# Kernel optimization log

Measured on AMD Instinct MI355X. Metric: run time of the kernel, lower is better.

## Reference

```python
import jax, jax.numpy as jnp
import numpy as np

N_NODES = 50000
N_EDGES = 800000
IN_DIM = 256
OUT_DIM = 64


def setup_inputs() -> dict:
    key = jax.random.key(0)
    k1, k2, k3, k4, k5 = jax.random.split(key, 5)
    h = jax.random.normal(k1, (N_NODES, IN_DIM), dtype=jnp.float32)
    # fc: Linear(in_dim, out_dim, bias=False) -> weight shape [out_dim, in_dim]
    W_fc = jax.random.normal(k2, (OUT_DIM, IN_DIM), dtype=jnp.float32) / np.sqrt(IN_DIM)
    # attn_fc: Linear(2*out_dim, 1, bias=False) -> weight shape [1, 2*out_dim]
    W_attn = jax.random.normal(k3, (1, 2 * OUT_DIM), dtype=jnp.float32) / np.sqrt(2 * OUT_DIM)
    src = jax.random.randint(k4, (N_EDGES,), 0, N_NODES, dtype=jnp.int64 if jax.config.read('jax_enable_x64') else jnp.int32).astype(jnp.int32)
    dst = jax.random.randint(k5, (N_EDGES,), 0, N_NODES, dtype=jnp.int32)
    return {"h": h, "W_fc": W_fc, "W_attn": W_attn, "src": src, "dst": dst}


def reference(h, W_fc, W_attn, src, dst):
    # z = self.fc(h)
    z = h @ W_fc.T                              # [N, D]
    # edge_attention: e = leaky_relu(attn_fc(cat(z_src, z_dst)))
    z_src = z[src]                              # [E, D] gather
    z_dst = z[dst]                              # [E, D] gather
    z2 = jnp.concatenate([z_src, z_dst], axis=1)  # [E, 2D]
    e = jax.nn.leaky_relu(z2 @ W_attn.T)[:, 0]  # [E], torch default slope 0.01
    # reduce_func: segment softmax over incoming edges per dst node
    n = h.shape[0]
    m = jax.ops.segment_max(e, dst, num_segments=n)        # [N] per-node max
    e_exp = jnp.exp(e - m[dst])                             # [E] stable exp
    denom = jax.ops.segment_sum(e_exp, dst, num_segments=n)  # [N]
    alpha = e_exp / jnp.maximum(denom, 1e-16)[dst]          # [E]
    # h' = sum_j alpha_ij * z_j
    out = jax.ops.segment_sum(alpha[:, None] * z_src, dst, num_segments=n)  # [N, D]
    return out
```

## Files before the change

### kernel.cpp

```cpp
#include <hip/hip_runtime.h>

#define N_NODES 50000
#define N_EDGES 800000
#define IN_DIM  256
#define OUT_DIM 64
#define BINW    128
#define NBINS   512
#define NBINS_USED ((N_NODES + BINW - 1) / BINW)
#define PB      112
#define CH4     ((N_EDGES / 4 + PB - 1) / PB)
#define NB_GEMM ((N_NODES + 63) / 64)
#define GRID_FUSED 896

typedef _Float16 f16;
typedef __attribute__((ext_vector_type(4))) _Float16 f16x4;
typedef __attribute__((ext_vector_type(8))) _Float16 f16x8;
typedef __attribute__((ext_vector_type(4))) float f32x4;


__global__ __launch_bounds__(256) void k_prep(const float* __restrict__ W,
                                              f16* __restrict__ Wh,
                                              int* __restrict__ binCount) {
    int idx = blockIdx.x * 256 + threadIdx.x;
    if (idx < (OUT_DIM * IN_DIM) / 4) {
        float4 v = ((const float4*)W)[idx];
        f16x4 p = { (f16)v.x, (f16)v.y, (f16)v.z, (f16)v.w };
        ((f16x4*)Wh)[idx] = p;
    }
    if (idx < NBINS) binCount[idx] = 0;
}

__global__ __launch_bounds__(256) void k_fused(const float* __restrict__ h,
                                               const f16* __restrict__ Wh,
                                               const float* __restrict__ Wa,
                                               const int* __restrict__ dst,
                                               f16* __restrict__ z,
                                               float* __restrict__ a_src,
                                               float* __restrict__ a_dst,
                                               int* __restrict__ binCount,
                                               int* __restrict__ base) {
    __shared__ __align__(16) f16 Al[64 * 128];
    const int g = blockIdx.x;
    const int t = threadIdx.x;

    if ((g & 7) == 7) {
        int* hist = (int*)Al;
        const int pb = g >> 3;
        for (int b = t; b < NBINS; b += 256) hist[b] = 0;
        __syncthreads();
        const int s4 = pb * CH4;
        const int e4 = min(s4 + CH4, N_EDGES / 4);
        for (int i4 = s4 + t; i4 < e4; i4 += 256) {
            int4 dv = ((const int4*)dst)[i4];
            atomicAdd(&hist[dv.x >> 7], 1);
            atomicAdd(&hist[dv.y >> 7], 1);
            atomicAdd(&hist[dv.z >> 7], 1);
            atomicAdd(&hist[dv.w >> 7], 1);
        }
        __syncthreads();
        for (int b = t; b < NBINS; b += 256) {
            int c = hist[b];
            if (c) base[pb * NBINS + b] = atomicAdd(&binCount[b], c);
        }
        return;
    }

    const int gemm_id = g - (g >> 3);
    if (gemm_id >= NB_GEMM) return;

    const int row0  = gemm_id * 64;
    const int lane  = t & 63;
    const int wid   = t >> 6;
    const int cl    = lane & 15;
    const int khalf = lane >> 4;

    f32x4 acc[4] = {};

    for (int kc = 0; kc < IN_DIM; kc += 128) {
        #pragma unroll
        for (int i = 0; i < 8; ++i) {
            int f   = i * 256 + t;
            int row = f >> 5, slot = f & 31;
            float4 v = make_float4(0.f, 0.f, 0.f, 0.f);
            if (row0 + row < N_NODES)
                v = *(const float4*)&h[(size_t)(row0 + row) * IN_DIM + kc + slot * 4];
            f16x4 p = { (f16)v.x, (f16)v.y, (f16)v.z, (f16)v.w };
            *(f16x4*)&Al[(row * 128 + slot * 4) ^ ((row & 7) << 3)] = p;
        }
        __syncthreads();

        #pragma unroll
        for (int ks = 0; ks < 4; ++ks) {
            const int arow = wid * 16 + cl;
            const int ak   = ks * 32 + khalf * 8;
            f16x8 a = *(const f16x8*)&Al[(arow * 128 + ak) ^ ((arow & 7) << 3)];
            #pragma unroll
            for (int ct = 0; ct < 4; ++ct) {
                const int col = ct * 16 + cl;
                const int bk  = kc + ks * 32 + khalf * 8;
                f16x8 b = *(const f16x8*)&Wh[col * 256 + bk];
                acc[ct] = __builtin_amdgcn_mfma_f32_16x16x32_f16(a, b, acc[ct], 0, 0, 0);
            }
        }
        __syncthreads();
    }

    const int rbase = row0 + wid * 16 + khalf * 4;
    #pragma unroll
    for (int ct = 0; ct < 4; ++ct) {
        #pragma unroll
        for (int r = 0; r < 4; ++r) {
            int row = rbase + r;
            if (row < N_NODES)
                z[(size_t)row * OUT_DIM + ct * 16 + cl] = (f16)acc[ct][r];
        }
    }

    float wa1[4], wa2[4];
    #pragma unroll
    for (int ct = 0; ct < 4; ++ct) {
        wa1[ct] = Wa[ct * 16 + cl];
        wa2[ct] = Wa[64 + ct * 16 + cl];
    }
    #pragma unroll
    for (int r = 0; r < 4; ++r) {
        float s1 = 0.f, s2 = 0.f;
        #pragma unroll
        for (int ct = 0; ct < 4; ++ct) {
            s1 += acc[ct][r] * wa1[ct];
            s2 += acc[ct][r] * wa2[ct];
        }
        #pragma unroll
        for (int off = 1; off < 16; off <<= 1) {
            s1 += __shfl_xor(s1, off);
            s2 += __shfl_xor(s2, off);
        }
        int row = rbase + r;
        if (cl == 0 && row < N_NODES) {
            a_src[row] = s1;
            a_dst[row] = s2;
        }
    }
}

__global__ __launch_bounds__(64) void k_binscan(const int* __restrict__ binCount,
                                                int* __restrict__ binStart) {
    const int lane = threadIdx.x;
    int vals[8];
    int run = 0;
    #pragma unroll
    for (int i = 0; i < 8; ++i) {
        int c = binCount[lane * 8 + i];
        vals[i] = run;
        run += c;
    }
    int incl = run;
    #pragma unroll
    for (int off = 1; off < 64; off <<= 1) {
        int u = __shfl_up(incl, off);
        if (lane >= off) incl += u;
    }
    const int lex = incl - run;
    #pragma unroll
    for (int i = 0; i < 8; ++i) binStart[lane * 8 + i] = lex + vals[i];
}

__global__ __launch_bounds__(256) void k_place(const int* __restrict__ src,
                                               const int* __restrict__ dst,
                                               const int* __restrict__ binStart,
                                               const int* __restrict__ base,
                                               int* __restrict__ ebuf) {
    __shared__ int cursor[NBINS];
    const int pb = blockIdx.x;
    const int t  = threadIdx.x;
    for (int b = t; b < NBINS; b += 256)
        cursor[b] = binStart[b] + base[pb * NBINS + b];
    __syncthreads();
    const int s4 = pb * CH4;
    const int e4 = min(s4 + CH4, N_EDGES / 4);
    for (int i4 = s4 + t; i4 < e4; i4 += 256) {
        int4 dv = ((const int4*)dst)[i4];
        int4 sv = ((const int4*)src)[i4];
        int slot;
        slot = atomicAdd(&cursor[dv.x >> 7], 1); ebuf[slot] = (sv.x << 7) | (dv.x & 127);
        slot = atomicAdd(&cursor[dv.y >> 7], 1); ebuf[slot] = (sv.y << 7) | (dv.y & 127);
        slot = atomicAdd(&cursor[dv.z >> 7], 1); ebuf[slot] = (sv.z << 7) | (dv.z & 127);
        slot = atomicAdd(&cursor[dv.w >> 7], 1); ebuf[slot] = (sv.w << 7) | (dv.w & 127);
    }
}

__global__ __launch_bounds__(256) void k_place2(const int* __restrict__ ebuf,
                                                const int* __restrict__ binStart,
                                                const int* __restrict__ binCount,
                                                int* __restrict__ csr_src,
                                                int* __restrict__ rowptr) {
    __shared__ int cnt[BINW];
    __shared__ int cur[BINW];
    const int b  = blockIdx.x;
    const int t  = threadIdx.x;
    const int node0  = b * BINW;
    const int estart = binStart[b];
    const int ecnt   = binCount[b];

    if (t < BINW) cnt[t] = 0;
    __syncthreads();

    for (int i = t; i < ecnt; i += 256)
        atomicAdd(&cnt[ebuf[estart + i] & (BINW - 1)], 1);
    __syncthreads();

    if (t < 64) {
        int v0 = cnt[t], v1 = cnt[t + 64];
        int i0 = v0;
        #pragma unroll
        for (int off = 1; off < 64; off <<= 1) {
            int u = __shfl_up(i0, off);
            if (t >= off) i0 += u;
        }
        int tot0 = __shfl(i0, 63);
        int i1 = v1;
        #pragma unroll
        for (int off = 1; off < 64; off <<= 1) {
            int u = __shfl_up(i1, off);
            if (t >= off) i1 += u;
        }
        int e0 = i0 - v0;
        int e1 = tot0 + i1 - v1;
        cur[t]      = e0;
        cur[t + 64] = e1;
        if (node0 + t <= N_NODES)      rowptr[node0 + t]      = estart + e0;
        if (node0 + t + 64 <= N_NODES) rowptr[node0 + t + 64] = estart + e1;
    }
    __syncthreads();

    for (int i = t; i < ecnt; i += 256) {
        int pk = ebuf[estart + i];
        int ld = pk & (BINW - 1);
        int p  = atomicAdd(&cur[ld], 1);
        csr_src[estart + p] = pk >> 7;
    }
}

__global__ __launch_bounds__(256) void k_aggregate(const int* __restrict__ rowptr,
                                                   const int* __restrict__ csr_src,
                                                   const float* __restrict__ a_src,
                                                   const float* __restrict__ a_dst,
                                                   const f16* __restrict__ z,
                                                   float* __restrict__ out) {
    __shared__ float2 buf[4][64];
    const int wid  = threadIdx.x >> 6;
    const int lane = threadIdx.x & 63;
    const int node = blockIdx.x * 4 + wid;
    if (node >= N_NODES) return;

    const int beg = rowptr[node];
    const int end = rowptr[node + 1];
    const int deg = end - beg;
    const float adst = a_dst[node];

    const int grp = lane >> 4;
    const int cl  = lane & 15;
    float dn = 0.0f;
    float4 acc4 = make_float4(0.f, 0.f, 0.f, 0.f);

    if (deg <= 64) {
        int s = 0;
        float w = 0.0f;
        if (lane < deg) {
            s = csr_src[beg + lane];
            float u = a_src[s] + adst;
            u = u > 0.0f ? u : 0.01f * u;
            w = __expf(u);
        }
        dn = w;
        #pragma unroll
        for (int off = 32; off; off >>= 1) dn += __shfl_xor(dn, off);

        buf[wid][lane] = make_float2(w, __int_as_float(s));
        __builtin_amdgcn_wave_barrier();

        const int kmax = (deg + 3) & ~3;
        for (int k = 0; k < kmax; k += 4) {
            float2 p = buf[wid][k + grp];
            int   sk = __float_as_int(p.y);
            float wk = p.x;
            f16x4 zv = *(const f16x4*)&z[(size_t)sk * OUT_DIM + cl * 4];
            acc4.x = fmaf(wk, (float)zv[0], acc4.x);
            acc4.y = fmaf(wk, (float)zv[1], acc4.y);
            acc4.z = fmaf(wk, (float)zv[2], acc4.z);
            acc4.w = fmaf(wk, (float)zv[3], acc4.w);
        }
    } else {
        float mx = -INFINITY;
        for (int j = beg + lane; j < end; j += 64) {
            int s = csr_src[j];
            float u = a_src[s] + adst;
            u = u > 0.0f ? u : 0.01f * u;
            mx = fmaxf(mx, u);
        }
        #pragma unroll
        for (int off = 32; off; off >>= 1) mx = fmaxf(mx, __shfl_xor(mx, off));

        for (int base = beg; base < end; base += 64) {
            int rem = end - base; if (rem > 64) rem = 64;
            int s = 0; float w = 0.0f;
            if (lane < rem) {
                s = csr_src[base + lane];
                float u = a_src[s] + adst;
                u = u > 0.0f ? u : 0.01f * u;
                w = __expf(u - mx);
            }
            dn += w;
            __builtin_amdgcn_wave_barrier();
            buf[wid][lane] = make_float2(w, __int_as_float(s));
            __builtin_amdgcn_wave_barrier();

            const int kmax = (rem + 3) & ~3;
            for (int k = 0; k < kmax; k += 4) {
                float2 p = buf[wid][k + grp];
                int   sk = __float_as_int(p.y);
                float wk = p.x;
                f16x4 zv = *(const f16x4*)&z[(size_t)sk * OUT_DIM + cl * 4];
                acc4.x = fmaf(wk, (float)zv[0], acc4.x);
                acc4.y = fmaf(wk, (float)zv[1], acc4.y);
                acc4.z = fmaf(wk, (float)zv[2], acc4.z);
                acc4.w = fmaf(wk, (float)zv[3], acc4.w);
            }
            __builtin_amdgcn_wave_barrier();
        }
        #pragma unroll
        for (int off = 32; off; off >>= 1) dn += __shfl_xor(dn, off);
    }

    #pragma unroll
    for (int off = 16; off < 64; off <<= 1) {
        acc4.x += __shfl_xor(acc4.x, off);
        acc4.y += __shfl_xor(acc4.y, off);
        acc4.z += __shfl_xor(acc4.z, off);
        acc4.w += __shfl_xor(acc4.w, off);
    }

    if (lane < 16) {
        float inv = 1.0f / fmaxf(dn, 1e-16f);
        float4 o = make_float4(acc4.x * inv, acc4.y * inv, acc4.z * inv, acc4.w * inv);
        *(float4*)&out[(size_t)node * OUT_DIM + cl * 4] = o;
    }
}


extern "C" void kernel_launch(void* const* d_in, const int* in_sizes, int n_in,
                              void* d_out, int out_size, void* d_ws, size_t ws_size,
                              hipStream_t stream) {
    const float* h      = (const float*)d_in[0];
    const float* W_fc   = (const float*)d_in[1];
    const float* W_attn = (const float*)d_in[2];
    const int*   src    = (const int*)d_in[3];
    const int*   dst    = (const int*)d_in[4];
    float* out = (float*)d_out;

    f16*   z        = (f16*)d_ws;
    f16*   Wh       = z + (size_t)N_NODES * OUT_DIM;
    float* a_src    = (float*)(Wh + OUT_DIM * IN_DIM);
    float* a_dst    = a_src + N_NODES;
    int*   binCount = (int*)(a_dst + N_NODES);
    int*   binStart = binCount + NBINS;
    int*   rowptr   = binStart + NBINS;
    int*   base     = rowptr + (N_NODES + 1);
    int*   ebuf     = base + PB * NBINS;
    int*   csr_src  = ebuf + N_EDGES;

    k_prep<<<16, 256, 0, stream>>>(W_fc, Wh, binCount);
    k_fused<<<GRID_FUSED, 256, 0, stream>>>(h, Wh, W_attn, dst, z, a_src, a_dst, binCount, base);
    k_binscan<<<1, 64, 0, stream>>>(binCount, binStart);
    k_place<<<PB, 256, 0, stream>>>(src, dst, binStart, base, ebuf);
    k_place2<<<NBINS_USED, 256, 0, stream>>>(ebuf, binStart, binCount, csr_src, rowptr);
    k_aggregate<<<(N_NODES + 3) / 4, 256, 0, stream>>>(rowptr, csr_src, a_src, a_dst, z, out);
}
```

Baseline: 80.22 us.

## Drop binscan kernel, load GEMM A directly from global, widen aggregate gathers

Removes the separate single-block bin scan launch: k_place recomputes the exclusive scan of bin counts per block, and k_place2 computes its own start offset by summing the preceding bins. The fused GEMM no longer stages h through LDS with barriers; each lane loads its A fragment straight from global memory and converts it with packed RTZ conversion. The aggregate kernel switches from 16 lanes doing 4-wide f16 loads to 8 lanes doing 8-wide loads, so more edges are processed per iteration. These changes trade a launch and some LDS traffic for redundant scan work in every block and less coalesced global reads of h.

```diff
diff --git a/kernel.cpp b/kernel.cpp
--- a/kernel.cpp
+++ b/kernel.cpp
@@ -13,6 +13,7 @@
 #define GRID_FUSED 896
 
 typedef _Float16 f16;
+typedef __attribute__((ext_vector_type(2))) __fp16 hf16x2;
 typedef __attribute__((ext_vector_type(4))) _Float16 f16x4;
 typedef __attribute__((ext_vector_type(8))) _Float16 f16x8;
 typedef __attribute__((ext_vector_type(4))) float f32x4;
@@ -39,12 +40,11 @@
                                                float* __restrict__ a_dst,
                                                int* __restrict__ binCount,
                                                int* __restrict__ base) {
-    __shared__ __align__(16) f16 Al[64 * 128];
+    __shared__ int hist[NBINS];
     const int g = blockIdx.x;
     const int t = threadIdx.x;
 
     if ((g & 7) == 7) {
-        int* hist = (int*)Al;
         const int pb = g >> 3;
         for (int b = t; b < NBINS; b += 256) hist[b] = 0;
         __syncthreads();
@@ -74,35 +74,33 @@
     const int cl    = lane & 15;
     const int khalf = lane >> 4;
 
+    const int arow = row0 + wid * 16 + cl;
+    const bool rok = arow < N_NODES;
+    const float* hrow = h + (size_t)arow * IN_DIM;
+
     f32x4 acc[4] = {};
 
-    for (int kc = 0; kc < IN_DIM; kc += 128) {
-        #pragma unroll
-        for (int i = 0; i < 8; ++i) {
-            int f   = i * 256 + t;
-            int row = f >> 5, slot = f & 31;
-            float4 v = make_float4(0.f, 0.f, 0.f, 0.f);
-            if (row0 + row < N_NODES)
-                v = *(const float4*)&h[(size_t)(row0 + row) * IN_DIM + kc + slot * 4];
-            f16x4 p = { (f16)v.x, (f16)v.y, (f16)v.z, (f16)v.w };
-            *(f16x4*)&Al[(row * 128 + slot * 4) ^ ((row & 7) << 3)] = p;
-        }
-        __syncthreads();
-
-        #pragma unroll
-        for (int ks = 0; ks < 4; ++ks) {
-            const int arow = wid * 16 + cl;
-            const int ak   = ks * 32 + khalf * 8;
-            f16x8 a = *(const f16x8*)&Al[(arow * 128 + ak) ^ ((arow & 7) << 3)];
-            #pragma unroll
-            for (int ct = 0; ct < 4; ++ct) {
-                const int col = ct * 16 + cl;
-                const int bk  = kc + ks * 32 + khalf * 8;
-                f16x8 b = *(const f16x8*)&Wh[col * 256 + bk];
-                acc[ct] = __builtin_amdgcn_mfma_f32_16x16x32_f16(a, b, acc[ct], 0, 0, 0);
-            }
-        }
-        __syncthreads();
+    #pragma unroll 4
+    for (int kc = 0; kc < IN_DIM; kc += 32) {
+        const int k0 = kc + khalf * 8;
+        float4 va = make_float4(0.f, 0.f, 0.f, 0.f);
+        float4 vb = make_float4(0.f, 0.f, 0.f, 0.f);
+        if (rok) {
+            va = *(const float4*)&hrow[k0];
+            vb = *(const float4*)&hrow[k0 + 4];
+        }
+        union { hf16x2 h2[4]; f16x8 h8; } ua;
+        ua.h2[0] = __builtin_amdgcn_cvt_pkrtz(va.x, va.y);
+        ua.h2[1] = __builtin_amdgcn_cvt_pkrtz(va.z, va.w);
+        ua.h2[2] = __builtin_amdgcn_cvt_pkrtz(vb.x, vb.y);
+        ua.h2[3] = __builtin_amdgcn_cvt_pkrtz(vb.z, vb.w);
+        f16x8 a = ua.h8;
+        #pragma unroll
+        for (int ct = 0; ct < 4; ++ct) {
+            const int col = ct * 16 + cl;
+            f16x8 b = *(const f16x8*)&Wh[col * 256 + k0];
+            acc[ct] = __builtin_amdgcn_mfma_f32_16x16x32_f16(a, b, acc[ct], 0, 0, 0);
+        }
     }
 
     const int rbase = row0 + wid * 16 + khalf * 4;
@@ -143,39 +141,33 @@
     }
 }
 
-__global__ __launch_bounds__(64) void k_binscan(const int* __restrict__ binCount,
-                                                int* __restrict__ binStart) {
-    const int lane = threadIdx.x;
-    int vals[8];
-    int run = 0;
-    #pragma unroll
-    for (int i = 0; i < 8; ++i) {
-        int c = binCount[lane * 8 + i];
-        vals[i] = run;
-        run += c;
-    }
-    int incl = run;
-    #pragma unroll
-    for (int off = 1; off < 64; off <<= 1) {
-        int u = __shfl_up(incl, off);
-        if (lane >= off) incl += u;
-    }
-    const int lex = incl - run;
-    #pragma unroll
-    for (int i = 0; i < 8; ++i) binStart[lane * 8 + i] = lex + vals[i];
-}
-
 __global__ __launch_bounds__(256) void k_place(const int* __restrict__ src,
                                                const int* __restrict__ dst,
-                                               const int* __restrict__ binStart,
+                                               const int* __restrict__ binCount,
                                                const int* __restrict__ base,
                                                int* __restrict__ ebuf) {
     __shared__ int cursor[NBINS];
     const int pb = blockIdx.x;
     const int t  = threadIdx.x;
-    for (int b = t; b < NBINS; b += 256)
-        cursor[b] = binStart[b] + base[pb * NBINS + b];
-    __syncthreads();
+
+    if (t < 64) {
+        int vals[8]; int run = 0;
+        #pragma unroll
+        for (int i = 0; i < 8; ++i) { int c = binCount[t * 8 + i]; vals[i] = run; run += c; }
+        int incl = run;
+        #pragma unroll
+        for (int off = 1; off < 64; off <<= 1) {
+            int u = __shfl_up(incl, off);
+            if (t >= off) incl += u;
+        }
+        const int lex = incl - run;
+        #pragma unroll
+        for (int i = 0; i < 8; ++i) cursor[t * 8 + i] = lex + vals[i];
+    }
+    __syncthreads();
+    for (int b = t; b < NBINS; b += 256) cursor[b] += base[pb * NBINS + b];
+    __syncthreads();
+
     const int s4 = pb * CH4;
     const int e4 = min(s4 + CH4, N_EDGES / 4);
     for (int i4 = s4 + t; i4 < e4; i4 += 256) {
@@ -190,20 +182,27 @@
 }
 
 __global__ __launch_bounds__(256) void k_place2(const int* __restrict__ ebuf,
-                                                const int* __restrict__ binStart,
                                                 const int* __restrict__ binCount,
                                                 int* __restrict__ csr_src,
                                                 int* __restrict__ rowptr) {
     __shared__ int cnt[BINW];
     __shared__ int cur[BINW];
+    __shared__ int sh_estart;
     const int b  = blockIdx.x;
     const int t  = threadIdx.x;
-    const int node0  = b * BINW;
-    const int estart = binStart[b];
-    const int ecnt   = binCount[b];
-
+    const int node0 = b * BINW;
+    const int ecnt  = binCount[b];
+
+    if (t < 64) {
+        int partial = 0;
+        for (int i = t; i < b; i += 64) partial += binCount[i];
+        #pragma unroll
+        for (int off = 32; off; off >>= 1) partial += __shfl_xor(partial, off);
+        if (t == 0) sh_estart = partial;
+    }
     if (t < BINW) cnt[t] = 0;
     __syncthreads();
+    const int estart = sh_estart;
 
     for (int i = t; i < ecnt; i += 256)
         atomicAdd(&cnt[ebuf[estart + i] & (BINW - 1)], 1);
@@ -258,10 +257,10 @@
     const int deg = end - beg;
     const float adst = a_dst[node];
 
-    const int grp = lane >> 4;
-    const int cl  = lane & 15;
+    const int grp = lane >> 3;
+    const int cl  = lane & 7;
     float dn = 0.0f;
-    float4 acc4 = make_float4(0.f, 0.f, 0.f, 0.f);
+    float acc8[8] = {0.f, 0.f, 0.f, 0.f, 0.f, 0.f, 0.f, 0.f};
 
     if (deg <= 64) {
         int s = 0;
@@ -273,22 +272,19 @@
             w = __expf(u);
         }
         dn = w;
-        #pragma unroll
-        for (int off = 32; off; off >>= 1) dn += __shfl_xor(dn, off);
 
         buf[wid][lane] = make_float2(w, __int_as_float(s));
         __builtin_amdgcn_wave_barrier();
 
-        const int kmax = (deg + 3) & ~3;
-        for (int k = 0; k < kmax; k += 4) {
+        const int kmax = (deg + 7) & ~7;
+        for (int k = 0; k < kmax; k += 8) {
             float2 p = buf[wid][k + grp];
             int   sk = __float_as_int(p.y);
             float wk = p.x;
-            f16x4 zv = *(const f16x4*)&z[(size_t)sk * OUT_DIM + cl * 4];
-            acc4.x = fmaf(wk, (float)zv[0], acc4.x);
-            acc4.y = fmaf(wk, (float)zv[1], acc4.y);
-            acc4.z = fmaf(wk, (float)zv[2], acc4.z);
-            acc4.w = fmaf(wk, (float)zv[3], acc4.w);
+            f16x8 zv = *(const f16x8*)&z[(size_t)sk * OUT_DIM + cl * 8];
+            #pragma unroll
+            for (int j = 0; j < 8; ++j)
+                acc8[j] = fmaf(wk, (float)zv[j], acc8[j]);
         }
     } else {
         float mx = -INFINITY;
@@ -301,11 +297,11 @@
         #pragma unroll
         for (int off = 32; off; off >>= 1) mx = fmaxf(mx, __shfl_xor(mx, off));
 
-        for (int base = beg; base < end; base += 64) {
-            int rem = end - base; if (rem > 64) rem = 64;
+        for (int base_ = beg; base_ < end; base_ += 64) {
+            int rem = end - base_; if (rem > 64) rem = 64;
             int s = 0; float w = 0.0f;
             if (lane < rem) {
-                s = csr_src[base + lane];
+                s = csr_src[base_ + lane];
                 float u = a_src[s] + adst;
                 u = u > 0.0f ? u : 0.01f * u;
                 w = __expf(u - mx);
@@ -315,35 +311,35 @@
             buf[wid][lane] = make_float2(w, __int_as_float(s));
             __builtin_amdgcn_wave_barrier();
 
-            const int kmax = (rem + 3) & ~3;
-            for (int k = 0; k < kmax; k += 4) {
+            const int kmax = (rem + 7) & ~7;
+            for (int k = 0; k < kmax; k += 8) {
                 float2 p = buf[wid][k + grp];
                 int   sk = __float_as_int(p.y);
                 float wk = p.x;
-                f16x4 zv = *(const f16x4*)&z[(size_t)sk * OUT_DIM + cl * 4];
-                acc4.x = fmaf(wk, (float)zv[0], acc4.x);
-                acc4.y = fmaf(wk, (float)zv[1], acc4.y);
-                acc4.z = fmaf(wk, (float)zv[2], acc4.z);
-                acc4.w = fmaf(wk, (float)zv[3], acc4.w);
+                f16x8 zv = *(const f16x8*)&z[(size_t)sk * OUT_DIM + cl * 8];
+                #pragma unroll
+                for (int j = 0; j < 8; ++j)
+                    acc8[j] = fmaf(wk, (float)zv[j], acc8[j]);
             }
             __builtin_amdgcn_wave_barrier();
         }
-        #pragma unroll
-        for (int off = 32; off; off >>= 1) dn += __shfl_xor(dn, off);
-    }
-
-    #pragma unroll
-    for (int off = 16; off < 64; off <<= 1) {
-        acc4.x += __shfl_xor(acc4.x, off);
-        acc4.y += __shfl_xor(acc4.y, off);
-        acc4.z += __shfl_xor(acc4.z, off);
-        acc4.w += __shfl_xor(acc4.w, off);
-    }
-
-    if (lane < 16) {
+    }
+
+    #pragma unroll
+    for (int off = 32; off; off >>= 1) dn += __shfl_xor(dn, off);
+    #pragma unroll
+    for (int off = 8; off < 64; off <<= 1) {
+        #pragma unroll
+        for (int j = 0; j < 8; ++j)
+            acc8[j] += __shfl_xor(acc8[j], off);
+    }
+
+    if (lane < 8) {
         float inv = 1.0f / fmaxf(dn, 1e-16f);
-        float4 o = make_float4(acc4.x * inv, acc4.y * inv, acc4.z * inv, acc4.w * inv);
-        *(float4*)&out[(size_t)node * OUT_DIM + cl * 4] = o;
+        float4 o0 = make_float4(acc8[0] * inv, acc8[1] * inv, acc8[2] * inv, acc8[3] * inv);
+        float4 o1 = make_float4(acc8[4] * inv, acc8[5] * inv, acc8[6] * inv, acc8[7] * inv);
+        *(float4*)&out[(size_t)node * OUT_DIM + lane * 8]     = o0;
+        *(float4*)&out[(size_t)node * OUT_DIM + lane * 8 + 4] = o1;
     }
 }
 
@@ -363,16 +359,14 @@
     float* a_src    = (float*)(Wh + OUT_DIM * IN_DIM);
     float* a_dst    = a_src + N_NODES;
     int*   binCount = (int*)(a_dst + N_NODES);
-    int*   binStart = binCount + NBINS;
-    int*   rowptr   = binStart + NBINS;
+    int*   rowptr   = binCount + NBINS;
     int*   base     = rowptr + (N_NODES + 1);
     int*   ebuf     = base + PB * NBINS;
     int*   csr_src  = ebuf + N_EDGES;
 
     k_prep<<<16, 256, 0, stream>>>(W_fc, Wh, binCount);
     k_fused<<<GRID_FUSED, 256, 0, stream>>>(h, Wh, W_attn, dst, z, a_src, a_dst, binCount, base);
-    k_binscan<<<1, 64, 0, stream>>>(binCount, binStart);
-    k_place<<<PB, 256, 0, stream>>>(src, dst, binStart, base, ebuf);
-    k_place2<<<NBINS_USED, 256, 0, stream>>>(ebuf, binStart, binCount, csr_src, rowptr);
+    k_place<<<PB, 256, 0, stream>>>(src, dst, binCount, base, ebuf);
+    k_place2<<<NBINS_USED, 256, 0, stream>>>(ebuf, binCount, csr_src, rowptr);
     k_aggregate<<<(N_NODES + 3) / 4, 256, 0, stream>>>(rowptr, csr_src, a_src, a_dst, z, out);
 }
```

New measurement: 79.39 us. About the same (-1.0%).
